# Kernel tuning notes

Hardware: AMD Instinct MI355X
Metric: run time of the kernel (lower is better)

## Reference

```python
import jax, jax.numpy as jnp
import numpy as np

N = 8192
C_IN = 128
C_OUT = 128
E = 262144


def setup_inputs() -> dict:
    key = jax.random.key(0)
    ks = jax.random.split(key, 8)
    x = jax.random.normal(ks[0], (1, C_IN, N), dtype=jnp.float32)
    edge_index = jax.random.randint(ks[1], (2, E), 0, N, dtype=jnp.int64)
    adj_mat = jax.random.randint(ks[2], (N, N), 0, 2).astype(jnp.float32)
    # conv1: Conv1d(C_IN, C_OUT, k=1, bias=False) -> weight (C_OUT, C_IN)
    W1 = jax.random.normal(ks[3], (C_OUT, C_IN), dtype=jnp.float32) * (1.0 / np.sqrt(C_IN))
    # f1/f2: Conv1d(C_OUT, 1, k=1) -> weight (C_OUT,), bias scalar
    w_f1 = jax.random.normal(ks[4], (C_OUT,), dtype=jnp.float32) * (1.0 / np.sqrt(C_OUT))
    b_f1 = jnp.zeros((), dtype=jnp.float32)
    w_f2 = jax.random.normal(ks[5], (C_OUT,), dtype=jnp.float32) * (1.0 / np.sqrt(C_OUT))
    b_f2 = jnp.zeros((), dtype=jnp.float32)
    return {"x": x, "edge_index": edge_index, "adj_mat": adj_mat,
            "W1": W1, "w_f1": w_f1, "b_f1": b_f1, "w_f2": w_f2, "b_f2": b_f2}


def reference(x, edge_index, adj_mat, W1, w_f1, b_f1, w_f2, b_f2):
    # seq_fts = conv1(x): 1x1 conv == GEMM over channel dim. (C_OUT, N)
    seq_fts = jnp.einsum('oc,cn->on', W1, x[0])
    # f1/f2: 1x1 conv to single channel -> per-node attention scalars (N,)
    a1 = jnp.einsum('c,cn->n', w_f1, seq_fts) + b_f1
    a2 = jnp.einsum('c,cn->n', w_f2, seq_fts) + b_f2
    # logits = adj*f1 + adj*f2^T  (N, N)
    logits = adj_mat * a1[:, None] + adj_mat * a2[None, :]
    coefs = jax.nn.softmax(jax.nn.leaky_relu(logits, negative_slope=0.01), axis=-1)
    # vals = coefs @ seq_fts^T  (N, C_OUT)
    vals = jnp.matmul(coefs, seq_fts.T)
    return jax.nn.elu(vals)[None]  # (1, N, C_OUT)
```

## Files before the change

### kernel.cpp

```cpp
#include <hip/hip_runtime.h>
#include <hip/hip_bf16.h>


typedef short bf16x8 __attribute__((ext_vector_type(8)));
typedef float f32x4 __attribute__((ext_vector_type(4)));

static __device__ __forceinline__ short f2bf(float f) {
  union { float f; unsigned u; } v; v.f = f;
  unsigned r = v.u + 0x7fffu + ((v.u >> 16) & 1u);
  return (short)(r >> 16);
}

static __device__ __forceinline__ void gld16(const short* g, short* l) {
  __builtin_amdgcn_global_load_lds(
      (const __attribute__((address_space(1))) void*)g,
      (__attribute__((address_space(3))) void*)l, 16, 0, 0);
}

__global__ __launch_bounds__(256) void k1_seqfts(
    const float* __restrict__ x, const float* __restrict__ W1,
    const float* __restrict__ wf1, const float* __restrict__ wf2,
    short* __restrict__ FT, float* __restrict__ a1, float* __restrict__ a2) {
  const int cb = blockIdx.x & 7;
  const int nb = blockIdx.x >> 3;
  const int n = nb * 256 + threadIdx.x;
  float acc[16];
#pragma unroll
  for (int i = 0; i < 16; ++i) acc[i] = 0.f;
  const float* wrow = W1 + cb * 16 * 128;
#pragma unroll 4
  for (int c = 0; c < 128; ++c) {
    float xv = x[c * 8192 + n];
#pragma unroll
    for (int cc = 0; cc < 16; ++cc) acc[cc] = fmaf(wrow[cc * 128 + c], xv, acc[cc]);
  }
  float p1 = 0.f, p2 = 0.f;
#pragma unroll
  for (int cc = 0; cc < 16; ++cc) {
    int co = cb * 16 + cc;
    FT[co * 8192 + n] = f2bf(acc[cc]);
    p1 = fmaf(wf1[co], acc[cc], p1);
    p2 = fmaf(wf2[co], acc[cc], p2);
  }
  atomicAdd(&a1[n], p1);
  atomicAdd(&a2[n], p2);
}

__global__ __launch_bounds__(512, 2) void k2_attn(
    const float* __restrict__ adj, const short* __restrict__ FT,
    const float* __restrict__ a1, const float* __restrict__ a2,
    const float* __restrict__ b1p, const float* __restrict__ b2p,
    float* __restrict__ out) {
  __shared__ __align__(16) short Ftl[3][16384];
  __shared__ __align__(16) short Pl[2][4360];
  __shared__ float zl[32];

  const int t = threadIdx.x;
  const int l = t & 63;
  const int w = t >> 6;
  const int r = l & 15;
  const int kg = l >> 4;
  const int i0 = blockIdx.x * 32;

  const int prow = t >> 4;
  const int pcg = t & 15;
  const float af = a1[i0 + prow] + b1p[0] + b2p[0];
  const float* adjp = adj + (size_t)(i0 + prow) * 8192 + pcg * 8;
  const float* a2p = a2 + pcg * 8;

  const int swz = 8 * (r ^ ((w * 4 + kg) & 15));
  const short* fsrc0 = FT + (size_t)(0 + w * 4 + kg) * 8192 + swz;
  const short* fsrc1 = FT + (size_t)(32 + w * 4 + kg) * 8192 + swz;
  const short* fsrc2 = FT + (size_t)(64 + w * 4 + kg) * 8192 + swz;
  const short* fsrc3 = FT + (size_t)(96 + w * 4 + kg) * 8192 + swz;

  const int mt = w >> 2;
  const int ct0 = (w & 3) * 2;
  const int arow = mt * 16 + r;
  const int c0 = ct0 * 16 + r;

  f32x4 acc0 = {0.f, 0.f, 0.f, 0.f};
  f32x4 acc1 = {0.f, 0.f, 0.f, 0.f};
  float zacc = 0.f;

  auto STAGE = [&](int s) {
    const int kb = s * 128;
    short* fb = &Ftl[s % 3][w * 512];
    gld16(fsrc0 + kb, fb);
    gld16(fsrc1 + kb, fb + 4096);
    gld16(fsrc2 + kb, fb + 8192);
    gld16(fsrc3 + kb, fb + 12288);
  };

  auto build = [&](int buf, const f32x4& A0, const f32x4& A1,
                   const f32x4& Q0, const f32x4& Q1) {
    bf16x8 pv;
#pragma unroll
    for (int j = 0; j < 4; ++j) {
      float tt = af + Q0[j];
      float lr = fmaxf(tt, 0.01f * tt);
      float p = __expf(A0[j] * lr);
      zacc += p;
      pv[j] = f2bf(p);
    }
#pragma unroll
    for (int j = 0; j < 4; ++j) {
      float tt = af + Q1[j];
      float lr = fmaxf(tt, 0.01f * tt);
      float p = __expf(A1[j] * lr);
      zacc += p;
      pv[4 + j] = f2bf(p);
    }
    *(bf16x8*)&Pl[buf][prow * 136 + pcg * 8] = pv;
  };

  auto compute = [&](int pbuf, int fbuf) {
    const short* pb = &Pl[pbuf][arow * 136 + kg * 8];
    const short* fb = &Ftl[fbuf][0];
#pragma unroll
    for (int kt = 0; kt < 4; ++kt) {
      const int koff = (kg * 8 + kt * 32) ^ (r * 8);
      bf16x8 Af = *(const bf16x8*)(pb + kt * 32);
      bf16x8 B0 = *(const bf16x8*)(fb + c0 * 128 + koff);
      bf16x8 B1 = *(const bf16x8*)(fb + (c0 + 16) * 128 + koff);
      acc0 = __builtin_amdgcn_mfma_f32_16x16x32_bf16(Af, B0, acc0, 0, 0, 0);
      acc1 = __builtin_amdgcn_mfma_f32_16x16x32_bf16(Af, B1, acc1, 0, 0, 0);
    }
  };

  auto body = [&](int s, const f32x4& uA0, const f32x4& uA1,
                  const f32x4& uQ0, const f32x4& uQ1,
                  f32x4& fA0, f32x4& fA1, f32x4& fQ0, f32x4& fQ1) {
    if (s + 2 < 64) STAGE(s + 2);
    if (s + 2 < 64) {
      const int kb2 = (s + 2) * 128;
      fA0 = *(const f32x4*)(adjp + kb2);
      fA1 = *(const f32x4*)(adjp + kb2 + 4);
      fQ0 = *(const f32x4*)(a2p + kb2);
      fQ1 = *(const f32x4*)(a2p + kb2 + 4);
    }
    if (s + 1 < 64) build((s + 1) & 1, uA0, uA1, uQ0, uQ1);
    compute(s & 1, s % 3);
    asm volatile("s_waitcnt lgkmcnt(0)" ::: "memory");
    asm volatile("s_waitcnt vmcnt(8)" ::: "memory");
    __builtin_amdgcn_s_barrier();
  };

  STAGE(0);
  STAGE(1);
  f32x4 tA0 = *(const f32x4*)(adjp);
  f32x4 tA1 = *(const f32x4*)(adjp + 4);
  f32x4 tQ0 = *(const f32x4*)(a2p);
  f32x4 tQ1 = *(const f32x4*)(a2p + 4);
  f32x4 oA0 = *(const f32x4*)(adjp + 128);
  f32x4 oA1 = *(const f32x4*)(adjp + 132);
  f32x4 oQ0 = *(const f32x4*)(a2p + 128);
  f32x4 oQ1 = *(const f32x4*)(a2p + 132);
  build(0, tA0, tA1, tQ0, tQ1);
  f32x4 eA0 = {0, 0, 0, 0}, eA1 = {0, 0, 0, 0}, eQ0 = {0, 0, 0, 0}, eQ1 = {0, 0, 0, 0};
  asm volatile("s_waitcnt lgkmcnt(0)" ::: "memory");
  asm volatile("s_waitcnt vmcnt(0)" ::: "memory");
  __builtin_amdgcn_s_barrier();

  for (int s = 0; s < 64; s += 2) {
    body(s, oA0, oA1, oQ0, oQ1, eA0, eA1, eQ0, eQ1);
    body(s + 1, eA0, eA1, eQ0, eQ1, oA0, oA1, oQ0, oQ1);
  }

  float zr = zacc;
  zr += __shfl_down(zr, 8, 16);
  zr += __shfl_down(zr, 4, 16);
  zr += __shfl_down(zr, 2, 16);
  zr += __shfl_down(zr, 1, 16);
  if (pcg == 0) zl[prow] = zr;
  __syncthreads();

#pragma unroll
  for (int q = 0; q < 4; ++q) {
    const int row = mt * 16 + kg * 4 + q;
    const float inv = 1.0f / zl[row];
    float v0 = acc0[q] * inv;
    v0 = v0 > 0.f ? v0 : __expf(v0) - 1.f;
    out[(size_t)(i0 + row) * 128 + c0] = v0;
    float v1 = acc1[q] * inv;
    v1 = v1 > 0.f ? v1 : __expf(v1) - 1.f;
    out[(size_t)(i0 + row) * 128 + c0 + 16] = v1;
  }
}

extern "C" void kernel_launch(void* const* d_in, const int* in_sizes, int n_in,
                              void* d_out, int out_size, void* d_ws, size_t ws_size,
                              hipStream_t stream) {
  const float* x   = (const float*)d_in[0];
  const float* adj = (const float*)d_in[2];
  const float* W1  = (const float*)d_in[3];
  const float* wf1 = (const float*)d_in[4];
  const float* b1  = (const float*)d_in[5];
  const float* wf2 = (const float*)d_in[6];
  const float* b2  = (const float*)d_in[7];
  float* out = (float*)d_out;

  short* FT = (short*)d_ws;
  float* a1 = (float*)((char*)d_ws + (size_t)2 * 1024 * 1024);
  float* a2 = a1 + 8192;

  hipMemsetAsync(a1, 0, 2 * 8192 * sizeof(float), stream);
  k1_seqfts<<<256, 256, 0, stream>>>(x, W1, wf1, wf2, FT, a1, a2);
  k2_attn<<<256, 512, 0, stream>>>(adj, FT, a1, a2, b1, b2, out);
}
```

Baseline: 120.8 us.

## Double K-step to 256 with two-stage LDS pipeline and single-buffered P tile

The attention kernel now processes 256 columns per pipeline step instead of 128, halving the step count and barrier overhead. The FT staging changes from a triple buffer of 128-wide tiles to a double buffer of 256-wide tiles with a new XOR swizzle. The P tile is single-buffered and rebuilt after an extra barrier once compute finishes. Launch bounds drop to one block per SIMD pair because LDS use roughly doubles, which lowers occupancy and latency hiding in exchange for fewer synchronisations.

Result: faster. 110.8 us (-8.3%).

```diff
diff --git a/kernel.cpp b/kernel.cpp
--- a/kernel.cpp
+++ b/kernel.cpp
@@ -46,13 +46,13 @@
   atomicAdd(&a2[n], p2);
 }
 
-__global__ __launch_bounds__(512, 2) void k2_attn(
+__global__ __launch_bounds__(512, 1) void k2_attn(
     const float* __restrict__ adj, const short* __restrict__ FT,
     const float* __restrict__ a1, const float* __restrict__ a2,
     const float* __restrict__ b1p, const float* __restrict__ b2p,
     float* __restrict__ out) {
-  __shared__ __align__(16) short Ftl[3][16384];
-  __shared__ __align__(16) short Pl[2][4360];
+  __shared__ __align__(16) short Ftl[2][32768];
+  __shared__ __align__(16) short Pl[8192];
   __shared__ float zl[32];
 
   const int t = threadIdx.x;
@@ -67,12 +67,12 @@
   const float af = a1[i0 + prow] + b1p[0] + b2p[0];
   const float* adjp = adj + (size_t)(i0 + prow) * 8192 + pcg * 8;
   const float* a2p = a2 + pcg * 8;
-
-  const int swz = 8 * (r ^ ((w * 4 + kg) & 15));
-  const short* fsrc0 = FT + (size_t)(0 + w * 4 + kg) * 8192 + swz;
-  const short* fsrc1 = FT + (size_t)(32 + w * 4 + kg) * 8192 + swz;
-  const short* fsrc2 = FT + (size_t)(64 + w * 4 + kg) * 8192 + swz;
-  const short* fsrc3 = FT + (size_t)(96 + w * 4 + kg) * 8192 + swz;
+  const int psw = (prow & 15) << 1;
+  const int pw0 = prow * 256 + ((pcg ^ psw) << 3);
+  const int pw1 = prow * 256 + (((pcg + 16) ^ psw) << 3);
+
+  const int chalf = l >> 5;
+  const int kslot = l & 31;
 
   const int mt = w >> 2;
   const int ct0 = (w & 3) * 2;
@@ -84,24 +84,27 @@
   float zacc = 0.f;
 
   auto STAGE = [&](int s) {
-    const int kb = s * 128;
-    short* fb = &Ftl[s % 3][w * 512];
-    gld16(fsrc0 + kb, fb);
-    gld16(fsrc1 + kb, fb + 4096);
-    gld16(fsrc2 + kb, fb + 8192);
-    gld16(fsrc3 + kb, fb + 12288);
-  };
-
-  auto build = [&](int buf, const f32x4& A0, const f32x4& A1,
-                   const f32x4& Q0, const f32x4& Q1) {
-    bf16x8 pv;
+#pragma unroll
+    for (int i = 0; i < 8; ++i) {
+      const int c = i * 16 + w * 2 + chalf;
+      const short* src = FT + (size_t)c * 8192 + s * 256 +
+                         ((kslot ^ ((c & 15) << 1)) << 3);
+      short* dst = &Ftl[s & 1][(i * 16 + w * 2) * 256];
+      gld16(src, dst);
+    }
+  };
+
+  auto build = [&](const f32x4& A0, const f32x4& A1, const f32x4& B0,
+                   const f32x4& B1, const f32x4& Q0, const f32x4& Q1,
+                   const f32x4& R0, const f32x4& R1) {
+    bf16x8 pv0, pv1;
 #pragma unroll
     for (int j = 0; j < 4; ++j) {
       float tt = af + Q0[j];
       float lr = fmaxf(tt, 0.01f * tt);
       float p = __expf(A0[j] * lr);
       zacc += p;
-      pv[j] = f2bf(p);
+      pv0[j] = f2bf(p);
     }
 #pragma unroll
     for (int j = 0; j < 4; ++j) {
@@ -109,62 +112,97 @@
       float lr = fmaxf(tt, 0.01f * tt);
       float p = __expf(A1[j] * lr);
       zacc += p;
-      pv[4 + j] = f2bf(p);
-    }
-    *(bf16x8*)&Pl[buf][prow * 136 + pcg * 8] = pv;
-  };
-
-  auto compute = [&](int pbuf, int fbuf) {
-    const short* pb = &Pl[pbuf][arow * 136 + kg * 8];
-    const short* fb = &Ftl[fbuf][0];
-#pragma unroll
-    for (int kt = 0; kt < 4; ++kt) {
-      const int koff = (kg * 8 + kt * 32) ^ (r * 8);
-      bf16x8 Af = *(const bf16x8*)(pb + kt * 32);
-      bf16x8 B0 = *(const bf16x8*)(fb + c0 * 128 + koff);
-      bf16x8 B1 = *(const bf16x8*)(fb + (c0 + 16) * 128 + koff);
+      pv0[4 + j] = f2bf(p);
+    }
+#pragma unroll
+    for (int j = 0; j < 4; ++j) {
+      float tt = af + R0[j];
+      float lr = fmaxf(tt, 0.01f * tt);
+      float p = __expf(B0[j] * lr);
+      zacc += p;
+      pv1[j] = f2bf(p);
+    }
+#pragma unroll
+    for (int j = 0; j < 4; ++j) {
+      float tt = af + R1[j];
+      float lr = fmaxf(tt, 0.01f * tt);
+      float p = __expf(B1[j] * lr);
+      zacc += p;
+      pv1[4 + j] = f2bf(p);
+    }
+    *(bf16x8*)&Pl[pw0] = pv0;
+    *(bf16x8*)&Pl[pw1] = pv1;
+  };
+
+  auto compute = [&](int s) {
+    const short* pb = Pl + arow * 256;
+    const short* fb = &Ftl[s & 1][0];
+#pragma unroll
+    for (int kt = 0; kt < 8; ++kt) {
+      const int sl = (((kt * 4 + kg) ^ (r << 1)) << 3);
+      bf16x8 Af = *(const bf16x8*)(pb + sl);
+      bf16x8 B0 = *(const bf16x8*)(fb + c0 * 256 + sl);
+      bf16x8 B1 = *(const bf16x8*)(fb + (c0 + 16) * 256 + sl);
       acc0 = __builtin_amdgcn_mfma_f32_16x16x32_bf16(Af, B0, acc0, 0, 0, 0);
       acc1 = __builtin_amdgcn_mfma_f32_16x16x32_bf16(Af, B1, acc1, 0, 0, 0);
     }
   };
 
-  auto body = [&](int s, const f32x4& uA0, const f32x4& uA1,
-                  const f32x4& uQ0, const f32x4& uQ1,
-                  f32x4& fA0, f32x4& fA1, f32x4& fQ0, f32x4& fQ1) {
-    if (s + 2 < 64) STAGE(s + 2);
-    if (s + 2 < 64) {
-      const int kb2 = (s + 2) * 128;
-      fA0 = *(const f32x4*)(adjp + kb2);
-      fA1 = *(const f32x4*)(adjp + kb2 + 4);
-      fQ0 = *(const f32x4*)(a2p + kb2);
-      fQ1 = *(const f32x4*)(a2p + kb2 + 4);
-    }
-    if (s + 1 < 64) build((s + 1) & 1, uA0, uA1, uQ0, uQ1);
-    compute(s & 1, s % 3);
+  auto body = [&](int s, const f32x4& uA0, const f32x4& uA1, const f32x4& uB0,
+                  const f32x4& uB1, const f32x4& uQ0, const f32x4& uQ1,
+                  const f32x4& uR0, const f32x4& uR1, f32x4& fA0, f32x4& fA1,
+                  f32x4& fB0, f32x4& fB1, f32x4& fQ0, f32x4& fQ1, f32x4& fR0,
+                  f32x4& fR1) {
+    if (s + 1 < 32) STAGE(s + 1);
+    __builtin_amdgcn_sched_barrier(0);
+    if (s + 2 < 32) {
+      const float* ap = adjp + (s + 2) * 256;
+      fA0 = *(const f32x4*)(ap);
+      fA1 = *(const f32x4*)(ap + 4);
+      fB0 = *(const f32x4*)(ap + 128);
+      fB1 = *(const f32x4*)(ap + 132);
+      const float* qp = a2p + (s + 2) * 256;
+      fQ0 = *(const f32x4*)(qp);
+      fQ1 = *(const f32x4*)(qp + 4);
+      fR0 = *(const f32x4*)(qp + 128);
+      fR1 = *(const f32x4*)(qp + 132);
+    }
+    compute(s);
+    __builtin_amdgcn_s_barrier();
+    if (s + 1 < 32) build(uA0, uA1, uB0, uB1, uQ0, uQ1, uR0, uR1);
     asm volatile("s_waitcnt lgkmcnt(0)" ::: "memory");
     asm volatile("s_waitcnt vmcnt(8)" ::: "memory");
     __builtin_amdgcn_s_barrier();
   };
 
   STAGE(0);
-  STAGE(1);
-  f32x4 tA0 = *(const f32x4*)(adjp);
-  f32x4 tA1 = *(const f32x4*)(adjp + 4);
-  f32x4 tQ0 = *(const f32x4*)(a2p);
-  f32x4 tQ1 = *(const f32x4*)(a2p + 4);
-  f32x4 oA0 = *(const f32x4*)(adjp + 128);
-  f32x4 oA1 = *(const f32x4*)(adjp + 132);
-  f32x4 oQ0 = *(const f32x4*)(a2p + 128);
-  f32x4 oQ1 = *(const f32x4*)(a2p + 132);
-  build(0, tA0, tA1, tQ0, tQ1);
-  f32x4 eA0 = {0, 0, 0, 0}, eA1 = {0, 0, 0, 0}, eQ0 = {0, 0, 0, 0}, eQ1 = {0, 0, 0, 0};
+  __builtin_amdgcn_sched_barrier(0);
+  f32x4 eA0 = *(const f32x4*)(adjp);
+  f32x4 eA1 = *(const f32x4*)(adjp + 4);
+  f32x4 eB0 = *(const f32x4*)(adjp + 128);
+  f32x4 eB1 = *(const f32x4*)(adjp + 132);
+  f32x4 eQ0 = *(const f32x4*)(a2p);
+  f32x4 eQ1 = *(const f32x4*)(a2p + 4);
+  f32x4 eR0 = *(const f32x4*)(a2p + 128);
+  f32x4 eR1 = *(const f32x4*)(a2p + 132);
+  f32x4 oA0 = *(const f32x4*)(adjp + 256);
+  f32x4 oA1 = *(const f32x4*)(adjp + 260);
+  f32x4 oB0 = *(const f32x4*)(adjp + 384);
+  f32x4 oB1 = *(const f32x4*)(adjp + 388);
+  f32x4 oQ0 = *(const f32x4*)(a2p + 256);
+  f32x4 oQ1 = *(const f32x4*)(a2p + 260);
+  f32x4 oR0 = *(const f32x4*)(a2p + 384);
+  f32x4 oR1 = *(const f32x4*)(a2p + 388);
+  build(eA0, eA1, eB0, eB1, eQ0, eQ1, eR0, eR1);
   asm volatile("s_waitcnt lgkmcnt(0)" ::: "memory");
-  asm volatile("s_waitcnt vmcnt(0)" ::: "memory");
+  asm volatile("s_waitcnt vmcnt(8)" ::: "memory");
   __builtin_amdgcn_s_barrier();
 
-  for (int s = 0; s < 64; s += 2) {
-    body(s, oA0, oA1, oQ0, oQ1, eA0, eA1, eQ0, eQ1);
-    body(s + 1, eA0, eA1, eQ0, eQ1, oA0, oA1, oQ0, oQ1);
+  for (int s = 0; s < 32; s += 2) {
+    body(s, oA0, oA1, oB0, oB1, oQ0, oQ1, oR0, oR1,
+         eA0, eA1, eB0, eB1, eQ0, eQ1, eR0, eR1);
+    body(s + 1, eA0, eA1, eB0, eB1, eQ0, eQ1, eR0, eR1,
+         oA0, oA1, oB0, oB1, oQ0, oQ1, oR0, oR1);
   }
 
   float zr = zacc;
```
